# Kernel tuning notes

Measured on AMD Instinct MI355X. Metric: run time of the kernel, lower is better.

## Reference

```python
import jax, jax.numpy as jnp
import numpy as np

GROUPS = 8
EPS = 1e-3  # keras GroupNormalization default epsilon


def group_norm(x, gamma, beta):
    # x: [B, H, W, C], channels-last, normalize over (H, W, C//G) per group
    B, H, W, C = x.shape
    g = x.reshape(B, H, W, GROUPS, C // GROUPS)
    mean = g.mean(axis=(1, 2, 4), keepdims=True)
    var = g.var(axis=(1, 2, 4), keepdims=True)
    g = (g - mean) * jax.lax.rsqrt(var + EPS)
    return g.reshape(B, H, W, C) * gamma + beta


def setup_inputs() -> dict:
    key = jax.random.key(0)
    ks = jax.random.split(key, 6)
    B, H, W, C = 4, 64, 64, 256
    s = 1.0 / np.sqrt(C)
    return {
        "x": jax.random.normal(ks[0], (B, H, W, C), jnp.float32),
        "gn_gamma": jnp.ones((C,), jnp.float32),
        "gn_beta": jnp.zeros((C,), jnp.float32),
        "Wq": jax.random.normal(ks[1], (C, C), jnp.float32) * s,
        "bq": jnp.zeros((C,), jnp.float32),
        "Wk": jax.random.normal(ks[2], (C, C), jnp.float32) * s,
        "bk": jnp.zeros((C,), jnp.float32),
        "Wv": jax.random.normal(ks[3], (C, C), jnp.float32) * s,
        "bv": jnp.zeros((C,), jnp.float32),
        "Wp": jax.random.normal(ks[4], (C, C), jnp.float32) * s,
        "bp": jnp.zeros((C,), jnp.float32),
    }


def reference(x, gn_gamma, gn_beta, Wq, bq, Wk, bk, Wv, bv, Wp, bp):
    B, H, W, C = x.shape
    scale = jnp.float32(C) ** -0.5
    xn = group_norm(x, gn_gamma, gn_beta)  # note: residual uses NORMALIZED input (as in source)
    xf = xn.reshape(B, H * W, C)           # flatten spatial -> [B, N, C]
    q = xf @ Wq + bq
    k = xf @ Wk + bk
    v = xf @ Wv + bv
    attn = jnp.einsum('bnc,bmc->bnm', q, k) * scale  # [B, N, N]
    attn = jax.nn.softmax(attn, axis=-1)
    out = jnp.einsum('bnm,bmc->bnc', attn, v)
    out = out @ Wp + bp
    return xn + out.reshape(B, H, W, C)
```

## Files before the change

### kernel.cpp

```cpp
#include <hip/hip_runtime.h>
#include <hip/hip_bf16.h>

typedef __bf16 bf16x8 __attribute__((ext_vector_type(8)));
typedef __bf16 bf16x4 __attribute__((ext_vector_type(4)));
typedef float f32x4 __attribute__((ext_vector_type(4)));
typedef float f32x16 __attribute__((ext_vector_type(16)));

#define MFMA16(a,b,c) __builtin_amdgcn_mfma_f32_16x16x32_bf16((a),(b),(c),0,0,0)
#define MFMA32(a,b,c) __builtin_amdgcn_mfma_f32_32x32x16_bf16((a),(b),(c),0,0,0)

__device__ __forceinline__ void gload_lds16(const void* g, void* l) {
    __builtin_amdgcn_global_load_lds((const __attribute__((address_space(1))) unsigned int*)g,
                                     (__attribute__((address_space(3))) unsigned int*)l, 16, 0, 0);
}

__global__ __launch_bounds__(256) void gn_stats1(const float* __restrict__ x,
                                                 float* __restrict__ pstats) {
    int blk = blockIdx.x;
    int bg = blk >> 4, sl = blk & 15;
    int b = bg >> 3, g = bg & 7;
    const float* base = x + ((size_t)b * 4096 + sl * 256) * 256 + g * 32;
    float s = 0.f, s2 = 0.f;
    for (int i = threadIdx.x; i < 2048; i += 256) {
        int pos = i >> 3, f4 = i & 7;
        float4 v = *(const float4*)(base + (size_t)pos * 256 + f4 * 4);
        s  += v.x + v.y + v.z + v.w;
        s2 += v.x * v.x + v.y * v.y + v.z * v.z + v.w * v.w;
    }
    for (int off = 32; off; off >>= 1) {
        s  += __shfl_down(s, off);
        s2 += __shfl_down(s2, off);
    }
    __shared__ float red[8];
    int wave = threadIdx.x >> 6, lane = threadIdx.x & 63;
    if (lane == 0) { red[wave] = s; red[4 + wave] = s2; }
    __syncthreads();
    if (threadIdx.x == 0) {
        pstats[blk * 2]     = red[0] + red[1] + red[2] + red[3];
        pstats[blk * 2 + 1] = red[4] + red[5] + red[6] + red[7];
    }
}

__global__ void gn_stats2(const float* __restrict__ pstats, float* __restrict__ stats) {
    int bg = threadIdx.x;
    if (bg < 32) {
        float S = 0.f, S2 = 0.f;
        for (int sl = 0; sl < 16; sl++) {
            S  += pstats[(bg * 16 + sl) * 2];
            S2 += pstats[(bg * 16 + sl) * 2 + 1];
        }
        const float invN = 1.f / 131072.f;
        float mean = S * invN;
        float var = S2 * invN - mean * mean;
        stats[bg * 2] = mean;
        stats[bg * 2 + 1] = rsqrtf(var + 1e-3f);
    }
}

__global__ __launch_bounds__(256) void gn_norm(const float* __restrict__ x,
                                               const float* __restrict__ gamma,
                                               const float* __restrict__ beta,
                                               const float* __restrict__ stats,
                                               float* __restrict__ xn_f32,
                                               __bf16* __restrict__ xn_bf) {
    size_t idx = (size_t)blockIdx.x * 256 + threadIdx.x;
    int c4 = (int)(idx & 63);
    int row = (int)(idx >> 6);
    int b = row >> 12;
    int g = c4 >> 3;
    float mean = stats[(b * 8 + g) * 2];
    float rstd = stats[(b * 8 + g) * 2 + 1];
    float4 xv = ((const float4*)x)[idx];
    float4 ga = ((const float4*)gamma)[c4];
    float4 be = ((const float4*)beta)[c4];
    float4 r;
    r.x = (xv.x - mean) * rstd * ga.x + be.x;
    r.y = (xv.y - mean) * rstd * ga.y + be.y;
    r.z = (xv.z - mean) * rstd * ga.z + be.z;
    r.w = (xv.w - mean) * rstd * ga.w + be.w;
    ((float4*)xn_f32)[idx] = r;
    bf16x4 o;
    o[0] = (__bf16)r.x; o[1] = (__bf16)r.y; o[2] = (__bf16)r.z; o[3] = (__bf16)r.w;
    *(bf16x4*)(xn_bf + idx * 4) = o;
}

__global__ __launch_bounds__(256) void prep_w(const float* __restrict__ Wq,
                                              const float* __restrict__ Wk,
                                              const float* __restrict__ Wv,
                                              const float* __restrict__ Wp,
                                              __bf16* __restrict__ wt) {
    int o = blockIdx.x * 256 + threadIdx.x;
    int w = o >> 16;
    int rem = o & 65535;
    int nt   = rem >> 12;
    int kf   = (rem >> 9) & 7;
    int quad = (rem >> 7) & 3;
    int l16  = (rem >> 3) & 15;
    int j    = rem & 7;
    int n = nt * 16 + l16;
    int k = kf * 32 + quad * 8 + j;
    const float* W = (w == 0) ? Wq : (w == 1) ? Wk : (w == 2) ? Wv : Wp;
    wt[o] = (__bf16)W[k * 256 + n];
}

__global__ __launch_bounds__(128, 2) void qkv_gemm(const __bf16* __restrict__ xn,
                                                   const __bf16* __restrict__ wt,
                                                   const float* __restrict__ bq,
                                                   const float* __restrict__ bk,
                                                   const float* __restrict__ bv,
                                                   __bf16* __restrict__ qout,
                                                   __bf16* __restrict__ kout,
                                                   __bf16* __restrict__ vtout) {
    __shared__ __bf16 atile[64][264];
    int w = blockIdx.z;
    const __bf16* Wl = wt + (size_t)w * 65536;
    int tid = threadIdx.x;
    int wave = tid >> 6, lane = tid & 63;
    int quad = lane >> 4, l16 = lane & 15;
    int m0 = blockIdx.x * 64;
    int ntbase = blockIdx.y * 8 + wave * 4;

#pragma unroll
    for (int i = 0; i < 16; i++) {
        int c = tid + 128 * i;
        int row = c >> 5, col = (c & 31) * 8;
        *(bf16x8*)&atile[row][col] = *(const bf16x8*)(xn + (size_t)(m0 + row) * 256 + col);
    }
    bf16x8 bfr[4][8];
#pragma unroll
    for (int ct = 0; ct < 4; ct++)
#pragma unroll
        for (int kf = 0; kf < 8; kf++)
            bfr[ct][kf] = *(const bf16x8*)(Wl + ((((size_t)(ntbase + ct) * 8 + kf) * 4 + quad) * 16 + l16) * 8);
    __syncthreads();

    f32x4 acc[4][4];
#pragma unroll
    for (int mt = 0; mt < 4; mt++)
#pragma unroll
        for (int ct = 0; ct < 4; ct++)
#pragma unroll
            for (int r = 0; r < 4; r++) acc[mt][ct][r] = 0.f;
#pragma unroll
    for (int kf = 0; kf < 8; kf++) {
        bf16x8 af[4];
#pragma unroll
        for (int mt = 0; mt < 4; mt++)
            af[mt] = *(const bf16x8*)&atile[mt * 16 + l16][kf * 32 + quad * 8];
#pragma unroll
        for (int mt = 0; mt < 4; mt++)
#pragma unroll
            for (int ct = 0; ct < 4; ct++)
                acc[mt][ct] = MFMA16(af[mt], bfr[ct][kf], acc[mt][ct]);
    }

    if (w == 2) {
        __syncthreads();
        __bf16 (*vtl)[70] = (__bf16(*)[70])atile;
#pragma unroll
        for (int mt = 0; mt < 4; mt++) {
#pragma unroll
            for (int ct = 0; ct < 4; ct++) {
                int cl = (wave * 4 + ct) * 16 + l16;
                float bias_v = bv[blockIdx.y * 128 + cl];
                bf16x4 pv;
#pragma unroll
                for (int r = 0; r < 4; r++) pv[r] = (__bf16)(acc[mt][ct][r] + bias_v);
                *(bf16x4*)&vtl[cl][mt * 16 + quad * 4] = pv;
            }
        }
        __syncthreads();
        int bb = m0 >> 12, n0g = m0 & 4095;
#pragma unroll
        for (int j = 0; j < 8; j++) {
            int chunk = tid + 128 * j;
            int cl = chunk >> 3, n8 = chunk & 7;
            *(bf16x8*)(vtout + ((size_t)(bb * 256 + blockIdx.y * 128 + cl)) * 4096 + n0g + n8 * 8)
                = *(const bf16x8*)&vtl[cl][n8 * 8];
        }
    } else {
        const float* bias = (w == 0) ? bq : bk;
        const float qscale = 0.09016844f;
#pragma unroll
        for (int mt = 0; mt < 4; mt++) {
#pragma unroll
            for (int ct = 0; ct < 4; ct++) {
                int c = (ntbase + ct) * 16 + l16;
                float bias_v = bias[c];
#pragma unroll
                for (int r = 0; r < 4; r++) {
                    int m = m0 + mt * 16 + quad * 4 + r;
                    float val = acc[mt][ct][r] + bias_v;
                    if (w == 0) qout[(size_t)m * 256 + c] = (__bf16)(val * qscale);
                    else        kout[(size_t)m * 256 + c] = (__bf16)val;
                }
            }
        }
    }
}

__global__ __launch_bounds__(256, 2) void flash_attn(const __bf16* __restrict__ q,
                                                     const __bf16* __restrict__ k,
                                                     const __bf16* __restrict__ vt,
                                                     __bf16* __restrict__ po,
                                                     float* __restrict__ ml) {
    __shared__ __align__(16) char smem[69632];
    __bf16 (*otr)[32][264] = (__bf16(*)[32][264])smem;

    const int tid = threadIdx.x;
    const int wave = tid >> 6, lane = tid & 63;
    const int l32 = lane & 31, h = lane >> 5;
    const int fid = blockIdx.x;
    const int cid = ((fid & 7) << 6) | (fid >> 3);
    const int qt  = cid & 31;
    const int ksb = cid >> 5;
    const int ks  = ksb & 3, b = ksb >> 2;
    const int row0 = qt * 128 + wave * 32;
    const size_t rowg0 = (size_t)b * 4096 + row0;

    const char*   kb = (const char*)(k + ((size_t)b * 4096 + ks * 1024) * 256);
    const __bf16* vb = vt + (size_t)b * 256 * 4096 + ks * 1024;

    int koff[4];
#pragma unroll
    for (int i = 0; i < 4; i++) {
        int P = wave * 256 + i * 64 + lane;
        int r = P >> 5, cp = P & 31;
        koff[i] = r * 512 + (cp ^ r) * 16;
    }
    const int kldsoff = wave * 4096;

    const int r4 = (lane >> 2) & 15, c4v = lane & 3;
    const int swl = (r4 ^ (r4 >> 2)) & 3;
    int voff[4];
#pragma unroll
    for (int i = 0; i < 4; i++) {
        int ch = wave * 64 + i * 16 + r4;
        voff[i] = ch * 4096 + (c4v ^ swl) * 8;
    }
    const int vldsoff = wave * 4096;

    bf16x8 qf[16];
    const __bf16* qbase = q + (rowg0 + l32) * 256 + h * 8;
#pragma unroll
    for (int s = 0; s < 16; s++) qf[s] = *(const bf16x8*)(qbase + s * 16);

    f32x16 acc[8];
#pragma unroll
    for (int ct = 0; ct < 8; ct++)
#pragma unroll
        for (int r = 0; r < 16; r++) acc[ct][r] = 0.f;
    float mi = -1e30f, li = 0.f;

#pragma unroll
    for (int i = 0; i < 4; i++)
        gload_lds16(kb + koff[i], smem + kldsoff + i * 1024);
#pragma unroll
    for (int i = 0; i < 4; i++)
        gload_lds16(vb + voff[i], smem + 32768 + vldsoff + i * 1024);
    asm volatile("s_waitcnt vmcnt(0)" ::: "memory");
    __builtin_amdgcn_sched_barrier(0);
    __builtin_amdgcn_s_barrier();

    for (int it = 0; it < 32; ++it) {
        const int cur = it & 1;
        const char* kcur = smem + (cur ? 16384 : 0);
        const char* vcur = smem + 32768 + (cur ? 16384 : 0);

        if (it + 1 < 32) {
            const char* kg = kb + (size_t)(it + 1) * 16384;
            char* kw = smem + (cur ? 0 : 16384);
#pragma unroll
            for (int i = 0; i < 4; i++)
                gload_lds16(kg + koff[i], kw + kldsoff + i * 1024);
            const int kn = (it + 1) * 32;
            char* vw = smem + 32768 + (cur ? 0 : 16384);
#pragma unroll
            for (int i = 0; i < 4; i++)
                gload_lds16(vb + voff[i] + kn, vw + vldsoff + i * 1024);
        }

        f32x16 s0_, s1_;
#pragma unroll
        for (int r = 0; r < 16; r++) { s0_[r] = 0.f; s1_[r] = 0.f; }
#pragma unroll
        for (int u = 0; u < 8; u++) {
            {
                int cl = 2 * u + h;
                bf16x8 ka = *(const bf16x8*)(kcur + l32 * 512 + ((cl ^ l32) << 4));
                s0_ = MFMA32(ka, qf[u], s0_);
            }
            {
                int cl = 2 * (u + 8) + h;
                bf16x8 ka = *(const bf16x8*)(kcur + l32 * 512 + ((cl ^ l32) << 4));
                s1_ = MFMA32(ka, qf[u + 8], s1_);
            }
        }
#pragma unroll
        for (int r = 0; r < 16; r++) s0_[r] += s1_[r];
        float mx = s0_[0];
#pragma unroll
        for (int r = 1; r < 16; r++) mx = fmaxf(mx, s0_[r]);
        mx = fmaxf(mx, __shfl_xor(mx, 32));
        if (__ballot(mx > mi + 8.0f)) {
            float mnew = fmaxf(mi, mx);
            float alpha = exp2f(mi - mnew);
#pragma unroll
            for (int ct = 0; ct < 8; ct++)
#pragma unroll
                for (int r = 0; r < 16; r++) acc[ct][r] *= alpha;
            li *= alpha;
            mi = mnew;
        }
        float rs = 0.f;
#pragma unroll
        for (int r = 0; r < 16; r++) { float p = exp2f(s0_[r] - mi); s0_[r] = p; rs += p; }
        rs += __shfl_xor(rs, 32);
        li += rs;
        bf16x8 pf0, pf1;
#pragma unroll
        for (int j = 0; j < 8; j++) { pf0[j] = (__bf16)s0_[j]; pf1[j] = (__bf16)s0_[8 + j]; }

        {
            const int sb = ((l32 ^ (l32 >> 2)) & 3) << 4;
            const char* vrow = vcur + l32 * 64 + h * 8;
            __builtin_amdgcn_s_setprio(1);
#pragma unroll
            for (int ct = 0; ct < 8; ct++) {
                const char* vr2 = vrow + ct * 2048;
                bf16x4 a00 = *(const bf16x4*)(vr2 + sb);
                bf16x4 a01 = *(const bf16x4*)(vr2 + (sb ^ 16));
                bf16x8 va0 = __builtin_shufflevector(a00, a01, 0, 1, 2, 3, 4, 5, 6, 7);
                acc[ct] = MFMA32(va0, pf0, acc[ct]);
                bf16x4 a10 = *(const bf16x4*)(vr2 + (sb ^ 32));
                bf16x4 a11 = *(const bf16x4*)(vr2 + (sb ^ 48));
                bf16x8 va1 = __builtin_shufflevector(a10, a11, 0, 1, 2, 3, 4, 5, 6, 7);
                acc[ct] = MFMA32(va1, pf1, acc[ct]);
            }
            __builtin_amdgcn_s_setprio(0);
        }

        asm volatile("s_waitcnt vmcnt(0) lgkmcnt(0)" ::: "memory");
        __builtin_amdgcn_sched_barrier(0);
        __builtin_amdgcn_s_barrier();
    }

#pragma unroll
    for (int ct = 0; ct < 8; ct++) {
#pragma unroll
        for (int pk = 0; pk < 4; pk++) {
            bf16x4 op;
            op[0] = (__bf16)acc[ct][pk * 4];     op[1] = (__bf16)acc[ct][pk * 4 + 1];
            op[2] = (__bf16)acc[ct][pk * 4 + 2]; op[3] = (__bf16)acc[ct][pk * 4 + 3];
            *(bf16x4*)&otr[wave][l32][ct * 32 + pk * 8 + h * 4] = op;
        }
    }
    if (lane < 32) {
        float2 v; v.x = mi; v.y = li;
        *(float2*)&ml[((size_t)ks * 16384 + rowg0 + l32) * 2] = v;
    }
    __syncthreads();
    __bf16* pobase = po + ((size_t)ks * 16384 + rowg0) * 256;
    const int rr = lane >> 1, half = lane & 1;
#pragma unroll
    for (int j = 0; j < 16; j++) {
        bf16x8 val = *(const bf16x8*)&otr[wave][rr][half * 128 + j * 8];
        *(bf16x8*)(pobase + (size_t)rr * 256 + half * 128 + j * 8) = val;
    }
}

__global__ __launch_bounds__(128, 2) void proj_gemm(const __bf16* __restrict__ po,
                                                    const float* __restrict__ ml,
                                                    const __bf16* __restrict__ wpl,
                                                    const float* __restrict__ bp,
                                                    float* __restrict__ out) {
    __shared__ __bf16 atile[64][264];
    int tid = threadIdx.x;
    int wave = tid >> 6, lane = tid & 63;
    int quad = lane >> 4, l16 = lane & 15;
    int m0 = blockIdx.x * 64;
    int ntbase = blockIdx.y * 8 + wave * 4;

#pragma unroll
    for (int i = 0; i < 16; i++) {
        int c = tid + 128 * i;
        int row = c >> 5, col8 = c & 31;
        int m = m0 + row;
        float mm[4], ll[4];
#pragma unroll
        for (int s = 0; s < 4; s++) {
            float2 v = *(const float2*)&ml[((size_t)s * 16384 + m) * 2];
            mm[s] = v.x; ll[s] = v.y;
        }
        float M = fmaxf(fmaxf(mm[0], mm[1]), fmaxf(mm[2], mm[3]));
        float den = 0.f, w[4];
#pragma unroll
        for (int s = 0; s < 4; s++) { w[s] = exp2f(mm[s] - M); den += ll[s] * w[s]; }
        float accv[8];
#pragma unroll
        for (int e = 0; e < 8; e++) accv[e] = 0.f;
#pragma unroll
        for (int s = 0; s < 4; s++) {
            bf16x8 pv = *(const bf16x8*)(po + ((size_t)s * 16384 + m) * 256 + col8 * 8);
#pragma unroll
            for (int e = 0; e < 8; e++) accv[e] += w[s] * (float)pv[e];
        }
        float rinv = 1.f / den;
        bf16x8 o;
#pragma unroll
        for (int e = 0; e < 8; e++) o[e] = (__bf16)(accv[e] * rinv);
        *(bf16x8*)&atile[row][col8 * 8] = o;
    }
    bf16x8 bfr[4][8];
#pragma unroll
    for (int ct = 0; ct < 4; ct++)
#pragma unroll
        for (int kf = 0; kf < 8; kf++)
            bfr[ct][kf] = *(const bf16x8*)(wpl + ((((size_t)(ntbase + ct) * 8 + kf) * 4 + quad) * 16 + l16) * 8);
    __syncthreads();

    f32x4 acc[4][4];
#pragma unroll
    for (int mt = 0; mt < 4; mt++)
#pragma unroll
        for (int ct = 0; ct < 4; ct++)
#pragma unroll
            for (int r = 0; r < 4; r++) acc[mt][ct][r] = 0.f;
#pragma unroll
    for (int kf = 0; kf < 8; kf++) {
        bf16x8 af[4];
#pragma unroll
        for (int mt = 0; mt < 4; mt++)
            af[mt] = *(const bf16x8*)&atile[mt * 16 + l16][kf * 32 + quad * 8];
#pragma unroll
        for (int mt = 0; mt < 4; mt++)
#pragma unroll
            for (int ct = 0; ct < 4; ct++)
                acc[mt][ct] = MFMA16(af[mt], bfr[ct][kf], acc[mt][ct]);
    }
#pragma unroll
    for (int mt = 0; mt < 4; mt++) {
#pragma unroll
        for (int ct = 0; ct < 4; ct++) {
            int c = (ntbase + ct) * 16 + l16;
            float bias_v = bp[c];
#pragma unroll
            for (int r = 0; r < 4; r++) {
                int m = m0 + mt * 16 + quad * 4 + r;
                size_t idx = (size_t)m * 256 + c;
                out[idx] = out[idx] + acc[mt][ct][r] + bias_v;
            }
        }
    }
}

extern "C" void kernel_launch(void* const* d_in, const int* in_sizes, int n_in,
                              void* d_out, int out_size, void* d_ws, size_t ws_size,
                              hipStream_t stream) {
    const float* x     = (const float*)d_in[0];
    const float* gamma = (const float*)d_in[1];
    const float* beta  = (const float*)d_in[2];
    const float* Wq    = (const float*)d_in[3];
    const float* bq    = (const float*)d_in[4];
    const float* Wk    = (const float*)d_in[5];
    const float* bk    = (const float*)d_in[6];
    const float* Wv    = (const float*)d_in[7];
    const float* bv    = (const float*)d_in[8];
    const float* Wp    = (const float*)d_in[9];
    const float* bp    = (const float*)d_in[10];
    float* out = (float*)d_out;

    char* ws = (char*)d_ws;
    __bf16* xn_bf   = (__bf16*)(ws);
    __bf16* wt      = (__bf16*)(ws + 8388608);
    __bf16* qbuf    = (__bf16*)(ws + 8912896);
    __bf16* kbuf    = (__bf16*)(ws + 17301504);
    __bf16* vtbuf   = (__bf16*)(ws + 25690112);
    __bf16* po      = (__bf16*)(ws + 34078720);
    float*  ml      = (float*)(ws + 67633152);
    float*  pstats  = (float*)(ws + 68157440);
    float*  gstats  = (float*)(ws + 68161536);

    gn_stats1<<<512, 256, 0, stream>>>(x, pstats);
    gn_stats2<<<1, 64, 0, stream>>>(pstats, gstats);
    gn_norm<<<4096, 256, 0, stream>>>(x, gamma, beta, gstats, out, xn_bf);
    prep_w<<<1024, 256, 0, stream>>>(Wq, Wk, Wv, Wp, wt);
    qkv_gemm<<<dim3(256, 2, 3), 128, 0, stream>>>(xn_bf, wt, bq, bk, bv, qbuf, kbuf, vtbuf);
    flash_attn<<<512, 256, 0, stream>>>(qbuf, kbuf, vtbuf, po, ml);
    proj_gemm<<<dim3(256, 2), 128, 0, stream>>>(po, ml, wt + 3 * 65536, bp, out);
}
```

Baseline: 255.9 us.

## Process two 32-row query tiles per wave in flash attention to reuse K/V

```diff
diff --git a/kernel.cpp b/kernel.cpp
--- a/kernel.cpp
+++ b/kernel.cpp
@@ -199,7 +199,7 @@
     }
 }
 
-__global__ __launch_bounds__(256, 2) void flash_attn(const __bf16* __restrict__ q,
+__global__ __launch_bounds__(256, 1) void flash_attn(const __bf16* __restrict__ q,
                                                      const __bf16* __restrict__ k,
                                                      const __bf16* __restrict__ vt,
                                                      __bf16* __restrict__ po,
@@ -211,11 +211,11 @@
     const int wave = tid >> 6, lane = tid & 63;
     const int l32 = lane & 31, h = lane >> 5;
     const int fid = blockIdx.x;
-    const int cid = ((fid & 7) << 6) | (fid >> 3);
-    const int qt  = cid & 31;
-    const int ksb = cid >> 5;
+    const int cid = ((fid & 7) << 5) | (fid >> 3);
+    const int qt  = cid & 15;
+    const int ksb = cid >> 4;
     const int ks  = ksb & 3, b = ksb >> 2;
-    const int row0 = qt * 128 + wave * 32;
+    const int row0 = qt * 256 + wave * 64;
     const size_t rowg0 = (size_t)b * 4096 + row0;
 
     const char*   kb = (const char*)(k + ((size_t)b * 4096 + ks * 1024) * 256);
@@ -240,17 +240,23 @@
     }
     const int vldsoff = wave * 4096;
 
-    bf16x8 qf[16];
-    const __bf16* qbase = q + (rowg0 + l32) * 256 + h * 8;
-#pragma unroll
-    for (int s = 0; s < 16; s++) qf[s] = *(const bf16x8*)(qbase + s * 16);
-
-    f32x16 acc[8];
+    bf16x8 qfA[16], qfB[16];
+    {
+        const __bf16* qa = q + (rowg0 + l32) * 256 + h * 8;
+        const __bf16* qb = q + (rowg0 + 32 + l32) * 256 + h * 8;
+#pragma unroll
+        for (int s = 0; s < 16; s++) {
+            qfA[s] = *(const bf16x8*)(qa + s * 16);
+            qfB[s] = *(const bf16x8*)(qb + s * 16);
+        }
+    }
+
+    f32x16 accA[8], accB[8];
 #pragma unroll
     for (int ct = 0; ct < 8; ct++)
 #pragma unroll
-        for (int r = 0; r < 16; r++) acc[ct][r] = 0.f;
-    float mi = -1e30f, li = 0.f;
+        for (int r = 0; r < 16; r++) { accA[ct][r] = 0.f; accB[ct][r] = 0.f; }
+    float miA = -1e30f, liA = 0.f, miB = -1e30f, liB = 0.f;
 
 #pragma unroll
     for (int i = 0; i < 4; i++)
@@ -280,46 +286,55 @@
                 gload_lds16(vb + voff[i] + kn, vw + vldsoff + i * 1024);
         }
 
-        f32x16 s0_, s1_;
-#pragma unroll
-        for (int r = 0; r < 16; r++) { s0_[r] = 0.f; s1_[r] = 0.f; }
-#pragma unroll
-        for (int u = 0; u < 8; u++) {
-            {
-                int cl = 2 * u + h;
-                bf16x8 ka = *(const bf16x8*)(kcur + l32 * 512 + ((cl ^ l32) << 4));
-                s0_ = MFMA32(ka, qf[u], s0_);
-            }
-            {
-                int cl = 2 * (u + 8) + h;
-                bf16x8 ka = *(const bf16x8*)(kcur + l32 * 512 + ((cl ^ l32) << 4));
-                s1_ = MFMA32(ka, qf[u + 8], s1_);
-            }
-        }
-#pragma unroll
-        for (int r = 0; r < 16; r++) s0_[r] += s1_[r];
-        float mx = s0_[0];
-#pragma unroll
-        for (int r = 1; r < 16; r++) mx = fmaxf(mx, s0_[r]);
-        mx = fmaxf(mx, __shfl_xor(mx, 32));
-        if (__ballot(mx > mi + 8.0f)) {
-            float mnew = fmaxf(mi, mx);
-            float alpha = exp2f(mi - mnew);
+        f32x16 sA, sB;
+#pragma unroll
+        for (int r = 0; r < 16; r++) { sA[r] = 0.f; sB[r] = 0.f; }
+#pragma unroll
+        for (int u = 0; u < 16; u++) {
+            int cl = 2 * u + h;
+            bf16x8 ka = *(const bf16x8*)(kcur + l32 * 512 + ((cl ^ l32) << 4));
+            sA = MFMA32(ka, qfA[u], sA);
+            sB = MFMA32(ka, qfB[u], sB);
+        }
+
+        float mxA = sA[0], mxB = sB[0];
+#pragma unroll
+        for (int r = 1; r < 16; r++) { mxA = fmaxf(mxA, sA[r]); mxB = fmaxf(mxB, sB[r]); }
+        mxA = fmaxf(mxA, __shfl_xor(mxA, 32));
+        mxB = fmaxf(mxB, __shfl_xor(mxB, 32));
+        if (__ballot(mxA > miA + 8.0f)) {
+            float mnew = fmaxf(miA, mxA);
+            float alpha = exp2f(miA - mnew);
 #pragma unroll
             for (int ct = 0; ct < 8; ct++)
 #pragma unroll
-                for (int r = 0; r < 16; r++) acc[ct][r] *= alpha;
-            li *= alpha;
-            mi = mnew;
-        }
-        float rs = 0.f;
-#pragma unroll
-        for (int r = 0; r < 16; r++) { float p = exp2f(s0_[r] - mi); s0_[r] = p; rs += p; }
-        rs += __shfl_xor(rs, 32);
-        li += rs;
-        bf16x8 pf0, pf1;
-#pragma unroll
-        for (int j = 0; j < 8; j++) { pf0[j] = (__bf16)s0_[j]; pf1[j] = (__bf16)s0_[8 + j]; }
+                for (int r = 0; r < 16; r++) accA[ct][r] *= alpha;
+            liA *= alpha; miA = mnew;
+        }
+        if (__ballot(mxB > miB + 8.0f)) {
+            float mnew = fmaxf(miB, mxB);
+            float alpha = exp2f(miB - mnew);
+#pragma unroll
+            for (int ct = 0; ct < 8; ct++)
+#pragma unroll
+                for (int r = 0; r < 16; r++) accB[ct][r] *= alpha;
+            liB *= alpha; miB = mnew;
+        }
+        float rsA = 0.f, rsB = 0.f;
+#pragma unroll
+        for (int r = 0; r < 16; r++) {
+            float pA = exp2f(sA[r] - miA); sA[r] = pA; rsA += pA;
+            float pB = exp2f(sB[r] - miB); sB[r] = pB; rsB += pB;
+        }
+        rsA += __shfl_xor(rsA, 32);
+        rsB += __shfl_xor(rsB, 32);
+        liA += rsA; liB += rsB;
+        bf16x8 pfA0, pfA1, pfB0, pfB1;
+#pragma unroll
+        for (int j = 0; j < 8; j++) {
+            pfA0[j] = (__bf16)sA[j]; pfA1[j] = (__bf16)sA[8 + j];
+            pfB0[j] = (__bf16)sB[j]; pfB1[j] = (__bf16)sB[8 + j];
+        }
 
         {
             const int sb = ((l32 ^ (l32 >> 2)) & 3) << 4;
@@ -331,11 +346,13 @@
                 bf16x4 a00 = *(const bf16x4*)(vr2 + sb);
                 bf16x4 a01 = *(const bf16x4*)(vr2 + (sb ^ 16));
                 bf16x8 va0 = __builtin_shufflevector(a00, a01, 0, 1, 2, 3, 4, 5, 6, 7);
-                acc[ct] = MFMA32(va0, pf0, acc[ct]);
+                accA[ct] = MFMA32(va0, pfA0, accA[ct]);
+                accB[ct] = MFMA32(va0, pfB0, accB[ct]);
                 bf16x4 a10 = *(const bf16x4*)(vr2 + (sb ^ 32));
                 bf16x4 a11 = *(const bf16x4*)(vr2 + (sb ^ 48));
                 bf16x8 va1 = __builtin_shufflevector(a10, a11, 0, 1, 2, 3, 4, 5, 6, 7);
-                acc[ct] = MFMA32(va1, pf1, acc[ct]);
+                accA[ct] = MFMA32(va1, pfA1, accA[ct]);
+                accB[ct] = MFMA32(va1, pfB1, accB[ct]);
             }
             __builtin_amdgcn_s_setprio(0);
         }
@@ -345,27 +362,53 @@
         __builtin_amdgcn_s_barrier();
     }
 
+    const int rr = lane >> 1, half = lane & 1;
 #pragma unroll
     for (int ct = 0; ct < 8; ct++) {
 #pragma unroll
         for (int pk = 0; pk < 4; pk++) {
             bf16x4 op;
-            op[0] = (__bf16)acc[ct][pk * 4];     op[1] = (__bf16)acc[ct][pk * 4 + 1];
-            op[2] = (__bf16)acc[ct][pk * 4 + 2]; op[3] = (__bf16)acc[ct][pk * 4 + 3];
+            op[0] = (__bf16)accA[ct][pk * 4];     op[1] = (__bf16)accA[ct][pk * 4 + 1];
+            op[2] = (__bf16)accA[ct][pk * 4 + 2]; op[3] = (__bf16)accA[ct][pk * 4 + 3];
             *(bf16x4*)&otr[wave][l32][ct * 32 + pk * 8 + h * 4] = op;
         }
     }
     if (lane < 32) {
-        float2 v; v.x = mi; v.y = li;
+        float2 v; v.x = miA; v.y = liA;
         *(float2*)&ml[((size_t)ks * 16384 + rowg0 + l32) * 2] = v;
     }
     __syncthreads();
-    __bf16* pobase = po + ((size_t)ks * 16384 + rowg0) * 256;
-    const int rr = lane >> 1, half = lane & 1;
-#pragma unroll
-    for (int j = 0; j < 16; j++) {
-        bf16x8 val = *(const bf16x8*)&otr[wave][rr][half * 128 + j * 8];
-        *(bf16x8*)(pobase + (size_t)rr * 256 + half * 128 + j * 8) = val;
+    {
+        __bf16* pobase = po + ((size_t)ks * 16384 + rowg0) * 256;
+#pragma unroll
+        for (int j = 0; j < 16; j++) {
+            bf16x8 val = *(const bf16x8*)&otr[wave][rr][half * 128 + j * 8];
+            *(bf16x8*)(pobase + (size_t)rr * 256 + half * 128 + j * 8) = val;
+        }
+    }
+    __syncthreads();
+#pragma unroll
+    for (int ct = 0; ct < 8; ct++) {
+#pragma unroll
+        for (int pk = 0; pk < 4; pk++) {
+            bf16x4 op;
+            op[0] = (__bf16)accB[ct][pk * 4];     op[1] = (__bf16)accB[ct][pk * 4 + 1];
+            op[2] = (__bf16)accB[ct][pk * 4 + 2]; op[3] = (__bf16)accB[ct][pk * 4 + 3];
+            *(bf16x4*)&otr[wave][l32][ct * 32 + pk * 8 + h * 4] = op;
+        }
+    }
+    if (lane < 32) {
+        float2 v; v.x = miB; v.y = liB;
+        *(float2*)&ml[((size_t)ks * 16384 + rowg0 + 32 + l32) * 2] = v;
+    }
+    __syncthreads();
+    {
+        __bf16* pobase = po + ((size_t)ks * 16384 + rowg0 + 32) * 256;
+#pragma unroll
+        for (int j = 0; j < 16; j++) {
+            bf16x8 val = *(const bf16x8*)&otr[wave][rr][half * 128 + j * 8];
+            *(bf16x8*)(pobase + (size_t)rr * 256 + half * 128 + j * 8) = val;
+        }
     }
 }
 
@@ -486,6 +529,6 @@
     gn_norm<<<4096, 256, 0, stream>>>(x, gamma, beta, gstats, out, xn_bf);
     prep_w<<<1024, 256, 0, stream>>>(Wq, Wk, Wv, Wp, wt);
     qkv_gemm<<<dim3(256, 2, 3), 128, 0, stream>>>(xn_bf, wt, bq, bk, bv, qbuf, kbuf, vtbuf);
-    flash_attn<<<512, 256, 0, stream>>>(qbuf, kbuf, vtbuf, po, ml);
+    flash_attn<<<256, 256, 0, stream>>>(qbuf, kbuf, vtbuf, po, ml);
     proj_gemm<<<dim3(256, 2), 128, 0, stream>>>(po, ml, wt + 3 * 65536, bp, out);
 }
```

Result: slower. 665.7 us (+160.1%).
